# Kernel tuning notes

Measured on AMD Instinct MI355X. Metric: run time of the kernel, lower is better.

The kernel has to match this reference:

```python
import jax, jax.numpy as jnp
import numpy as np

N_NODES = 100000
N_EDGES = 1600000
F_IN = 128
HEADS1, CH1 = 8, 16
N_CLASSES = 64
NEG_SLOPE = 0.2  # PyG GATConv default leaky-relu slope


def setup_inputs() -> dict:
    key = jax.random.key(0)
    ks = jax.random.split(key, 10)
    x = jax.random.normal(ks[0], (N_NODES, F_IN), dtype=jnp.float32)
    edge_index = jax.random.randint(ks[1], (2, N_EDGES), 0, N_NODES, dtype=jnp.int32)
    s1 = 1.0 / np.sqrt(F_IN)
    s2 = 1.0 / np.sqrt(HEADS1 * CH1)
    W1 = jax.random.normal(ks[2], (F_IN, HEADS1 * CH1), dtype=jnp.float32) * s1
    a_src1 = jax.random.normal(ks[3], (HEADS1, CH1), dtype=jnp.float32) * s2
    a_dst1 = jax.random.normal(ks[4], (HEADS1, CH1), dtype=jnp.float32) * s2
    b1 = jnp.zeros((HEADS1 * CH1,), dtype=jnp.float32)
    W2 = jax.random.normal(ks[5], (HEADS1 * CH1, N_CLASSES), dtype=jnp.float32) * s2
    a_src2 = jax.random.normal(ks[6], (1, N_CLASSES), dtype=jnp.float32) * 0.1
    a_dst2 = jax.random.normal(ks[7], (1, N_CLASSES), dtype=jnp.float32) * 0.1
    b2 = jnp.zeros((N_CLASSES,), dtype=jnp.float32)
    return {"x": x, "edge_index": edge_index, "W1": W1, "a_src1": a_src1,
            "a_dst1": a_dst1, "b1": b1, "W2": W2, "a_src2": a_src2,
            "a_dst2": a_dst2, "b2": b2}


def gat_layer(x, src, dst, W, a_src, a_dst, b, heads, ch, concat):
    # PyG GATConv (eval mode, self-loops already appended to src/dst).
    N = x.shape[0]
    h = (x @ W).reshape(N, heads, ch)                      # [N,H,C]
    asn = jnp.einsum('nhc,hc->nh', h, a_src)               # src attention term
    adn = jnp.einsum('nhc,hc->nh', h, a_dst)               # dst attention term
    e = jax.nn.leaky_relu(asn[src] + adn[dst], NEG_SLOPE)  # [E,H]
    emax = jax.ops.segment_max(e, dst, num_segments=N)     # per-dst max (self-loops guarantee nonempty)
    ee = jnp.exp(e - emax[dst])
    denom = jax.ops.segment_sum(ee, dst, num_segments=N)
    alpha = ee / denom[dst]                                # segment softmax over incoming edges
    msg = h[src] * alpha[:, :, None]                       # [E,H,C]
    out = jax.ops.segment_sum(msg, dst, num_segments=N)    # [N,H,C]
    out = out.reshape(N, heads * ch) if concat else out.mean(axis=1)
    return out + b


def reference(x, edge_index, W1, a_src1, a_dst1, b1, W2, a_src2, a_dst2, b2):
    N = x.shape[0]
    loop = jnp.arange(N, dtype=edge_index.dtype)
    src = jnp.concatenate([edge_index[0], loop])  # add self-loops (PyG default)
    dst = jnp.concatenate([edge_index[1], loop])
    h = gat_layer(x, src, dst, W1, a_src1, a_dst1, b1, HEADS1, CH1, True)
    h = jax.nn.elu(h)
    # F.dropout with training=False is identity (eval mode)
    out = gat_layer(h, src, dst, W2, a_src2, a_dst2, b2, 1, N_CLASSES, False)
    return jax.nn.log_softmax(out, axis=1)
```

## Files before the change

### kernel.cpp

```cpp
#include <hip/hip_runtime.h>

#define NN 100000
#define NE 1600000
#define EN (NE + NN)
#define FIN 128
#define H1 8
#define C1 16
#define F1 128
#define NC 64
#define NEG 0.2f

#define BSH 9
#define BKN 512
#define NBUK ((NN + BKN - 1) / BKN)
#define NBLK 256
#define CHUNK ((EN + NBLK - 1) / NBLK)
__device__ __forceinline__ int chunk_of_block(int b) {
  return (b & 7) * (NBLK / 8) + (b >> 3);
}

typedef unsigned short ushort_t;
typedef unsigned int uint_t;
typedef __attribute__((ext_vector_type(8))) short short8v;
typedef __attribute__((ext_vector_type(4))) float f32x4;
typedef __attribute__((ext_vector_type(2))) float f32x2;

union U8 { ushort_t u[8]; short8v v; uint4 q; };

__device__ __forceinline__ ushort_t f2bf(float f) {
  uint_t u = __builtin_bit_cast(uint_t, f);
  u += 0x7FFF + ((u >> 16) & 1);
  return (ushort_t)(u >> 16);
}
__device__ __forceinline__ float bflo(uint_t u) {
  return __builtin_bit_cast(float, u << 16);
}
__device__ __forceinline__ float bfhi(uint_t u) {
  return __builtin_bit_cast(float, u & 0xFFFF0000u);
}

#if __has_builtin(__builtin_amdgcn_cvt_pk_fp8_f32) && \
    __has_builtin(__builtin_amdgcn_cvt_pk_f32_fp8)
__device__ __forceinline__ uint_t fp8_pack4(float f0, float f1, float f2,
                                            float f3) {
  int p = 0;
  p = __builtin_amdgcn_cvt_pk_fp8_f32(f0, f1, p, false);
  p = __builtin_amdgcn_cvt_pk_fp8_f32(f2, f3, p, true);
  return (uint_t)p;
}
__device__ __forceinline__ void fp8_unpack4(uint_t w, float* o) {
  f32x2 d0 = __builtin_amdgcn_cvt_pk_f32_fp8((int)w, false);
  f32x2 d1 = __builtin_amdgcn_cvt_pk_f32_fp8((int)w, true);
  o[0] = d0.x; o[1] = d0.y; o[2] = d1.x; o[3] = d1.y;
}
#else
__device__ __forceinline__ uint_t fp8_enc1(float f) {
  uint_t u = __builtin_bit_cast(uint_t, f);
  uint_t s = (u >> 24) & 0x80u;
  int e = (int)((u >> 23) & 0xFF) - 127;
  if (e < -9) return s;
  if (e < -6) {
    float af = __builtin_bit_cast(float, u & 0x7FFFFFFFu);
    uint_t m = (uint_t)(af * 512.f + 0.5f);
    return s | m;
  }
  uint_t mant = u & 0x7FFFFF;
  uint_t keep = mant >> 20;
  uint_t rest = mant & 0xFFFFF;
  keep += (rest > 0x80000u) || (rest == 0x80000u && (keep & 1));
  uint_t ee = (uint_t)(e + 7);
  if (keep == 8) { keep = 0; ee += 1; }
  if (ee > 15 || (ee == 15 && keep > 6)) return s | 0x7E;
  return s | (ee << 3) | keep;
}
__device__ __forceinline__ float fp8_dec1(uint_t b) {
  uint_t s = (b & 0x80u) << 24;
  uint_t e = (b >> 3) & 15u, m = b & 7u;
  if (e == 0) {
    float v = (float)m * (1.0f / 512.0f);
    return __builtin_bit_cast(float, s | __builtin_bit_cast(uint_t, v));
  }
  return __builtin_bit_cast(float, s | ((e + 120u) << 23) | (m << 20));
}
__device__ __forceinline__ uint_t fp8_pack4(float f0, float f1, float f2,
                                            float f3) {
  return fp8_enc1(f0) | (fp8_enc1(f1) << 8) | (fp8_enc1(f2) << 16) |
         (fp8_enc1(f3) << 24);
}
__device__ __forceinline__ void fp8_unpack4(uint_t w, float* o) {
  o[0] = fp8_dec1(w & 0xFF); o[1] = fp8_dec1((w >> 8) & 0xFF);
  o[2] = fp8_dec1((w >> 16) & 0xFF); o[3] = fp8_dec1(w >> 24);
}
#endif

__global__ __launch_bounds__(512) void bucket_count_kernel(
    const int* __restrict__ dstA, int* __restrict__ cnt,
    const float* __restrict__ W1, const float* __restrict__ W2,
    ushort_t* __restrict__ WT1, ushort_t* __restrict__ WT2) {
  __shared__ int histL[NBUK];
  int b = blockIdx.x, t = threadIdx.x;
  int gid = b * 512 + t;
  if (gid < 128 * 128) {
    int n = gid >> 7, k = gid & 127;
    int c = (n & 15) * 8 + (n >> 4);
    WT1[gid] = f2bf(W1[k * 128 + c]);
  } else if (gid < 128 * 128 + 64 * 128) {
    int j = gid - 128 * 128;
    int n = j >> 7, k = j & 127;
    int c = (n & 15) * 4 + (n >> 4);
    WT2[j] = f2bf(W2[k * 64 + c]);
  }
  for (int i = t; i < NBUK; i += 512) histL[i] = 0;
  __syncthreads();
  int ch = chunk_of_block(b);
  int e0 = ch * CHUNK, e1 = min(e0 + CHUNK, EN);
  for (int e = e0 + t; e < e1; e += 512) {
    int d = (e < NE) ? dstA[e] : (e - NE);
    atomicAdd(&histL[d >> BSH], 1);
  }
  __syncthreads();
  for (int i = t; i < NBUK; i += 512) cnt[i * NBLK + ch] = histL[i];
}

__global__ __launch_bounds__(256) void bucket_scan_kernel(
    int* __restrict__ cnt, int* __restrict__ bucket_base) {
  __shared__ int colsum[NBUK];
  int t = threadIdx.x;
  if (t < NBUK) {
    int run = 0;
    int* c = cnt + t * NBLK;
    for (int b = 0; b < NBLK; ++b) { int v = c[b]; c[b] = run; run += v; }
    colsum[t] = run;
  }
  __syncthreads();
  if (t == 0) {
    int base = 0;
    for (int j = 0; j < NBUK; ++j) {
      bucket_base[j] = base;
      int v = colsum[j];
      colsum[j] = base;
      base += v;
    }
    bucket_base[NBUK] = base;
  }
  __syncthreads();
  if (t < NBUK) {
    int bb = colsum[t];
    int* c = cnt + t * NBLK;
    for (int b = 0; b < NBLK; ++b) c[b] += bb;
  }
}

__global__ __launch_bounds__(512) void scatter_gemm1_kernel(
    const int* __restrict__ srcA, const int* __restrict__ dstA,
    const int* __restrict__ cnt, int* __restrict__ staging,
    const float* __restrict__ X, const ushort_t* __restrict__ WT1,
    const float* __restrict__ a_src, const float* __restrict__ a_dst,
    uint2* __restrict__ h8, float* __restrict__ asn, float* __restrict__ adn,
    int nrows) {
  __shared__ int cur[NBUK];
  if (blockIdx.x < NBLK) {
    int b = blockIdx.x, t = threadIdx.x;
    int ch = chunk_of_block(b);
    for (int i = t; i < NBUK; i += 512) cur[i] = cnt[i * NBLK + ch];
    __syncthreads();
    int e0 = ch * CHUNK, e1 = min(e0 + CHUNK, EN);
    for (int e = e0 + t; e < e1; e += 512) {
      int s, d;
      if (e < NE) { s = srcA[e]; d = dstA[e]; } else { s = e - NE; d = s; }
      int pos = atomicAdd(&cur[d >> BSH], 1);
      staging[pos] = s | ((d & (BKN - 1)) << 17);
    }
    return;
  }
  const int tid = threadIdx.x;
  const int wave = tid >> 6, lane = tid & 63;
  const int row0 = (blockIdx.x - NBLK) * 128 + wave * 16;
  const int rlo = lane & 15, khi = lane >> 4;

  f32x4 acc[8];
#pragma unroll
  for (int n = 0; n < 8; ++n) acc[n] = (f32x4){0.f, 0.f, 0.f, 0.f};

#pragma unroll
  for (int ks = 0; ks < 4; ++ks) {
    const int kk = ks * 32 + khi * 8;
    int row = row0 + rlo;
    if (row >= nrows) row = nrows - 1;
    const float4* xp = (const float4*)(X + (size_t)row * 128 + kk);
    float4 u = xp[0], v = xp[1];
    U8 t;
    t.u[0] = f2bf(u.x); t.u[1] = f2bf(u.y); t.u[2] = f2bf(u.z); t.u[3] = f2bf(u.w);
    t.u[4] = f2bf(v.x); t.u[5] = f2bf(v.y); t.u[6] = f2bf(v.z); t.u[7] = f2bf(v.w);
    short8v a = t.v;
#pragma unroll
    for (int nf = 0; nf < 8; ++nf) {
      short8v b = *(const short8v*)(WT1 + (nf * 16 + rlo) * 128 + kk);
      acc[nf] = __builtin_amdgcn_mfma_f32_16x16x32_bf16(a, b, acc[nf], 0, 0, 0);
    }
  }
  const float4* as4 = (const float4*)a_src;
  const float4* ad4 = (const float4*)a_dst;
  float4 as0 = as4[rlo * 2], as1 = as4[rlo * 2 + 1];
  float4 ad0 = ad4[rlo * 2], ad1 = ad4[rlo * 2 + 1];
  int rbase = row0 + khi * 4;
#pragma unroll
  for (int r = 0; r < 4; ++r) {
    int row = rbase + r;
    bool ok = (row < nrows);
    uint2 pk;
    pk.x = fp8_pack4(acc[0][r], acc[1][r], acc[2][r], acc[3][r]);
    pk.y = fp8_pack4(acc[4][r], acc[5][r], acc[6][r], acc[7][r]);
    if (ok) h8[(size_t)row * 16 + rlo] = pk;
    float s = acc[0][r] * as0.x + acc[1][r] * as0.y +
              acc[2][r] * as0.z + acc[3][r] * as0.w +
              acc[4][r] * as1.x + acc[5][r] * as1.y +
              acc[6][r] * as1.z + acc[7][r] * as1.w;
    float d = acc[0][r] * ad0.x + acc[1][r] * ad0.y +
              acc[2][r] * ad0.z + acc[3][r] * ad0.w +
              acc[4][r] * ad1.x + acc[5][r] * ad1.y +
              acc[6][r] * ad1.z + acc[7][r] * ad1.w;
    s += __shfl_xor(s, 1);
    d += __shfl_xor(d, 1);
    if (ok && (rlo & 1) == 0) {
      asn[row * 8 + (rlo >> 1)] = s;
      adn[row * 8 + (rlo >> 1)] = d;
    }
  }
}

__global__ __launch_bounds__(512) void bucket_csr_kernel(
    const int* __restrict__ staging, const int* __restrict__ bucket_base,
    int* __restrict__ rp, int* __restrict__ col) {
  __shared__ int degL[BKN];
  __shared__ int exclL[BKN];
  __shared__ int sdata[2][BKN];
  int bk = blockIdx.x, t = threadIdx.x;
  int ebase = bucket_base[bk], eend = bucket_base[bk + 1];
  int ecnt = eend - ebase;
  degL[t] = 0;
  __syncthreads();
  for (int e = t; e < ecnt; e += 512)
    atomicAdd(&degL[staging[ebase + e] >> 17], 1);
  __syncthreads();
  int v = degL[t];
  sdata[0][t] = v;
  __syncthreads();
  int sp = 0;
  for (int off = 1; off < BKN; off <<= 1) {
    int val = sdata[sp][t];
    if (t >= off) val += sdata[sp][t - off];
    sdata[sp ^ 1][t] = val;
    __syncthreads();
    sp ^= 1;
  }
  int ex = sdata[sp][t] - v;
  exclL[t] = ex;
  int node = bk * BKN + t;
  if (node < NN) rp[node] = ebase + ex;
  if (bk == 0 && t == 0) rp[NN] = EN;
  __syncthreads();
  for (int e = t; e < ecnt; e += 512) {
    int pk = staging[ebase + e];
    int pos = atomicAdd(&exclL[pk >> 17], 1);
    col[ebase + pos] = pk & 0x1FFFF;
  }
}

__global__ __launch_bounds__(256) void mfma_gemm2_kernel(
    const ushort_t* __restrict__ X2, const ushort_t* __restrict__ WT2,
    const float* __restrict__ a_src, const float* __restrict__ a_dst,
    uint_t* __restrict__ h28, float* __restrict__ asn, float* __restrict__ adn,
    int nrows) {
  const int tid = threadIdx.x;
  const int wave = tid >> 6, lane = tid & 63;
  const int row0 = blockIdx.x * 64 + wave * 16;
  const int rlo = lane & 15, khi = lane >> 4;

  f32x4 acc[4];
#pragma unroll
  for (int n = 0; n < 4; ++n) acc[n] = (f32x4){0.f, 0.f, 0.f, 0.f};

#pragma unroll
  for (int ks = 0; ks < 4; ++ks) {
    const int kk = ks * 32 + khi * 8;
    int row = row0 + rlo;
    if (row >= nrows) row = nrows - 1;
    U8 t;
    t.q = *(const uint4*)(X2 + (size_t)row * 128 + kk);
    short8v a = t.v;
#pragma unroll
    for (int nf = 0; nf < 4; ++nf) {
      short8v b = *(const short8v*)(WT2 + (nf * 16 + rlo) * 128 + kk);
      acc[nf] = __builtin_amdgcn_mfma_f32_16x16x32_bf16(a, b, acc[nf], 0, 0, 0);
    }
  }
  float4 as = ((const float4*)a_src)[rlo];
  float4 ad = ((const float4*)a_dst)[rlo];
  int rbase = row0 + khi * 4;
#pragma unroll
  for (int r = 0; r < 4; ++r) {
    int row = rbase + r;
    bool ok = (row < nrows);
    uint_t pk = fp8_pack4(acc[0][r], acc[1][r], acc[2][r], acc[3][r]);
    if (ok) h28[(size_t)row * 16 + rlo] = pk;
    float s = acc[0][r] * as.x + acc[1][r] * as.y +
              acc[2][r] * as.z + acc[3][r] * as.w;
    float d = acc[0][r] * ad.x + acc[1][r] * ad.y +
              acc[2][r] * ad.z + acc[3][r] * ad.w;
    s += __shfl_xor(s, 1); s += __shfl_xor(s, 2);
    s += __shfl_xor(s, 4); s += __shfl_xor(s, 8);
    d += __shfl_xor(d, 1); d += __shfl_xor(d, 2);
    d += __shfl_xor(d, 4); d += __shfl_xor(d, 8);
    if (ok && rlo == 0) { asn[row] = s; adn[row] = d; }
  }
}

__global__ __launch_bounds__(256) void gather1_kernel(
    const int* __restrict__ rp, const int* __restrict__ col,
    const float* __restrict__ asn, const float* __restrict__ adn,
    const uint4* __restrict__ h8, const float* __restrict__ b1,
    ushort_t* __restrict__ x2) {
  int node = (blockIdx.x << 5) + (threadIdx.x >> 3);
  if (node >= NN) return;
  int lane = threadIdx.x & 7;
  float aD = adn[node * 8 + lane];
  int p = rp[node], p1 = rp[node + 1];
  float a[16];
#pragma unroll
  for (int j = 0; j < 16; ++j) a[j] = 0.f;
  float den = 0.f;

  for (; p + 1 < p1; p += 2) {
    int s0 = col[p], s1 = col[p + 1];
    float e0 = asn[s0 * 8 + lane] + aD;
    float e1 = asn[s1 * 8 + lane] + aD;
    uint4 q0 = h8[(size_t)s0 * 8 + lane];
    uint4 q1 = h8[(size_t)s1 * 8 + lane];
    e0 = e0 > 0.f ? e0 : NEG * e0;
    e1 = e1 > 0.f ? e1 : NEG * e1;
    float ee0 = __expf(e0), ee1 = __expf(e1);
    float d0[4], d1[4], d2[4], d3[4];
    fp8_unpack4(q0.x, d0); fp8_unpack4(q0.y, d1);
    fp8_unpack4(q0.z, d2); fp8_unpack4(q0.w, d3);
    float g0[4], g1[4], g2[4], g3[4];
    fp8_unpack4(q1.x, g0); fp8_unpack4(q1.y, g1);
    fp8_unpack4(q1.z, g2); fp8_unpack4(q1.w, g3);
#pragma unroll
    for (int j = 0; j < 4; ++j) {
      a[j]      += ee0 * d0[j] + ee1 * g0[j];
      a[4 + j]  += ee0 * d1[j] + ee1 * g1[j];
      a[8 + j]  += ee0 * d2[j] + ee1 * g2[j];
      a[12 + j] += ee0 * d3[j] + ee1 * g3[j];
    }
    den += ee0 + ee1;
  }
  if (p < p1) {
    int s0 = col[p];
    float e0 = asn[s0 * 8 + lane] + aD;
    uint4 q0 = h8[(size_t)s0 * 8 + lane];
    e0 = e0 > 0.f ? e0 : NEG * e0;
    float ee0 = __expf(e0);
    float d0[4], d1[4], d2[4], d3[4];
    fp8_unpack4(q0.x, d0); fp8_unpack4(q0.y, d1);
    fp8_unpack4(q0.z, d2); fp8_unpack4(q0.w, d3);
#pragma unroll
    for (int j = 0; j < 4; ++j) {
      a[j] += ee0 * d0[j];
      a[4 + j] += ee0 * d1[j];
      a[8 + j] += ee0 * d2[j];
      a[12 + j] += ee0 * d3[j];
    }
    den += ee0;
  }
  float inv = 1.f / den;
  const float4* b4 = (const float4*)b1;
  U8 t0, t1;
#pragma unroll
  for (int h = 0; h < 4; ++h) {
    float4 bv = b4[lane * 4 + h];
    float o0 = fmaf(a[h * 4 + 0], inv, bv.x);
    float o1 = fmaf(a[h * 4 + 1], inv, bv.y);
    float o2 = fmaf(a[h * 4 + 2], inv, bv.z);
    float o3 = fmaf(a[h * 4 + 3], inv, bv.w);
    o0 = o0 > 0.f ? o0 : __expf(o0) - 1.f;
    o1 = o1 > 0.f ? o1 : __expf(o1) - 1.f;
    o2 = o2 > 0.f ? o2 : __expf(o2) - 1.f;
    o3 = o3 > 0.f ? o3 : __expf(o3) - 1.f;
    U8& t = (h < 2) ? t0 : t1;
    int base = (h & 1) * 4;
    t.u[base + 0] = f2bf(o0); t.u[base + 1] = f2bf(o1);
    t.u[base + 2] = f2bf(o2); t.u[base + 3] = f2bf(o3);
  }
  uint4* xr = (uint4*)(x2 + (size_t)node * F1);
  xr[lane * 2 + 0] = t0.q;
  xr[lane * 2 + 1] = t1.q;
}

__global__ __launch_bounds__(256) void gather2_kernel(
    const int* __restrict__ rp, const int* __restrict__ col,
    const float* __restrict__ asn, const float* __restrict__ adn,
    const uint2* __restrict__ h28, const float* __restrict__ b2,
    float* __restrict__ out) {
  int node = (blockIdx.x << 5) + (threadIdx.x >> 3);
  if (node >= NN) return;
  int lane = threadIdx.x & 7;
  float aD = adn[node];
  int p = rp[node], p1 = rp[node + 1];
  float a[8];
#pragma unroll
  for (int j = 0; j < 8; ++j) a[j] = 0.f;
  float den = 0.f;

  for (; p + 1 < p1; p += 2) {
    int s0 = col[p], s1 = col[p + 1];
    float e0 = asn[s0] + aD;
    float e1 = asn[s1] + aD;
    uint2 q0 = h28[(size_t)s0 * 8 + lane];
    uint2 q1 = h28[(size_t)s1 * 8 + lane];
    e0 = e0 > 0.f ? e0 : NEG * e0;
    e1 = e1 > 0.f ? e1 : NEG * e1;
    float ee0 = __expf(e0), ee1 = __expf(e1);
    float d0[4], d1[4], g0[4], g1[4];
    fp8_unpack4(q0.x, d0); fp8_unpack4(q0.y, d1);
    fp8_unpack4(q1.x, g0); fp8_unpack4(q1.y, g1);
#pragma unroll
    for (int j = 0; j < 4; ++j) {
      a[j] += ee0 * d0[j] + ee1 * g0[j];
      a[4 + j] += ee0 * d1[j] + ee1 * g1[j];
    }
    den += ee0 + ee1;
  }
  if (p < p1) {
    int s0 = col[p];
    float e0 = asn[s0] + aD;
    uint2 q0 = h28[(size_t)s0 * 8 + lane];
    e0 = e0 > 0.f ? e0 : NEG * e0;
    float ee0 = __expf(e0);
    float d0[4], d1[4];
    fp8_unpack4(q0.x, d0); fp8_unpack4(q0.y, d1);
#pragma unroll
    for (int j = 0; j < 4; ++j) {
      a[j] += ee0 * d0[j];
      a[4 + j] += ee0 * d1[j];
    }
    den += ee0;
  }
  float inv = 1.f / den;
  float4 bv0 = ((const float4*)b2)[lane * 2 + 0];
  float4 bv1 = ((const float4*)b2)[lane * 2 + 1];
  float v[8];
  v[0] = fmaf(a[0], inv, bv0.x); v[1] = fmaf(a[1], inv, bv0.y);
  v[2] = fmaf(a[2], inv, bv0.z); v[3] = fmaf(a[3], inv, bv0.w);
  v[4] = fmaf(a[4], inv, bv1.x); v[5] = fmaf(a[5], inv, bv1.y);
  v[6] = fmaf(a[6], inv, bv1.z); v[7] = fmaf(a[7], inv, bv1.w);
  float m = v[0];
#pragma unroll
  for (int j = 1; j < 8; ++j) m = fmaxf(m, v[j]);
#pragma unroll
  for (int k = 1; k < 8; k <<= 1) m = fmaxf(m, __shfl_xor(m, k));
  float ex = 0.f;
#pragma unroll
  for (int j = 0; j < 8; ++j) ex += __expf(v[j] - m);
#pragma unroll
  for (int k = 1; k < 8; k <<= 1) ex += __shfl_xor(ex, k);
  float lse = m + __logf(ex);
  float4 r0 = {v[0] - lse, v[1] - lse, v[2] - lse, v[3] - lse};
  float4 r1 = {v[4] - lse, v[5] - lse, v[6] - lse, v[7] - lse};
  float4* orow = (float4*)(out + (size_t)node * NC);
  orow[lane * 2 + 0] = r0;
  orow[lane * 2 + 1] = r1;
}

extern "C" void kernel_launch(void* const* d_in, const int* in_sizes, int n_in,
                              void* d_out, int out_size, void* d_ws,
                              size_t ws_size, hipStream_t stream) {
  const float* x = (const float*)d_in[0];
  const int* edge_index = (const int*)d_in[1];
  const float* W1 = (const float*)d_in[2];
  const float* a_src1 = (const float*)d_in[3];
  const float* a_dst1 = (const float*)d_in[4];
  const float* b1 = (const float*)d_in[5];
  const float* W2 = (const float*)d_in[6];
  const float* a_src2 = (const float*)d_in[7];
  const float* a_dst2 = (const float*)d_in[8];
  const float* b2 = (const float*)d_in[9];
  float* out = (float*)d_out;
  float* ws = (float*)d_ws;

  ushort_t* x2b = (ushort_t*)ws;
  uint4* h8 = (uint4*)(ws + 6400000);
  uint2* h28 = (uint2*)(ws + 9600000);
  float* asn1 = ws + 11200000;
  float* adn1 = ws + 12000000;
  float* asn2 = ws + 12800000;
  float* adn2 = ws + 12900000;
  ushort_t* WT1 = (ushort_t*)(ws + 13000000);
  ushort_t* WT2 = (ushort_t*)(ws + 13010000);
  int* rp = (int*)(ws + 13020000);
  int* col = rp + NN + 1;
  int* staging = col + EN;
  int* cnt = staging + EN;
  int* bucket_base = cnt + NBUK * NBLK;

  const int* srcA = edge_index;
  const int* dstA = edge_index + NE;

  bucket_count_kernel<<<NBLK, 512, 0, stream>>>(dstA, cnt, W1, W2, WT1, WT2);
  bucket_scan_kernel<<<1, 256, 0, stream>>>(cnt, bucket_base);
  scatter_gemm1_kernel<<<NBLK + (NN + 127) / 128, 512, 0, stream>>>(
      srcA, dstA, cnt, staging, x, WT1, a_src1, a_dst1, (uint2*)h8, asn1, adn1,
      NN);
  bucket_csr_kernel<<<NBUK, 512, 0, stream>>>(staging, bucket_base, rp, col);
  gather1_kernel<<<(NN + 31) / 32, 256, 0, stream>>>(rp, col, asn1, adn1, h8,
                                                     b1, x2b);
  mfma_gemm2_kernel<<<(NN + 63) / 64, 256, 0, stream>>>(
      x2b, WT2, a_src2, a_dst2, (uint_t*)h28, asn2, adn2, NN);
  gather2_kernel<<<(NN + 31) / 32, 256, 0, stream>>>(rp, col, asn2, adn2, h28,
                                                     b2, out);
}
```

Measured before the change: 218.3 us.

## Fuse CSR bucket build with layer-1 gather and shrink buckets to 128 nodes

The bucket size drops from 512 to 128 nodes, so there are about 782 buckets, and the scan kernel now loops over buckets with a stride of 256. The per-bucket CSR construction is fused with the layer-1 attention gather. Each 512-thread block builds col for its 128 nodes, then aggregates them in two passes of 64 nodes, reading col from the just-written L2-hot region. This removes one kernel launch and a round-trip of col and rp through memory. In exchange, the single-block scan does more serial work on more columns, and the gather runs at block granularity with barriers that may reduce latency hiding.

```diff
diff --git a/kernel.cpp b/kernel.cpp
--- a/kernel.cpp
+++ b/kernel.cpp
@@ -10,8 +10,8 @@
 #define NC 64
 #define NEG 0.2f
 
-#define BSH 9
-#define BKN 512
+#define BSH 7
+#define BKN 128
 #define NBUK ((NN + BKN - 1) / BKN)
 #define NBLK 256
 #define CHUNK ((EN + NBLK - 1) / NBLK)
@@ -126,11 +126,11 @@
     int* __restrict__ cnt, int* __restrict__ bucket_base) {
   __shared__ int colsum[NBUK];
   int t = threadIdx.x;
-  if (t < NBUK) {
+  for (int j = t; j < NBUK; j += 256) {
     int run = 0;
-    int* c = cnt + t * NBLK;
+    int* c = cnt + j * NBLK;
     for (int b = 0; b < NBLK; ++b) { int v = c[b]; c[b] = run; run += v; }
-    colsum[t] = run;
+    colsum[j] = run;
   }
   __syncthreads();
   if (t == 0) {
@@ -144,9 +144,9 @@
     bucket_base[NBUK] = base;
   }
   __syncthreads();
-  if (t < NBUK) {
-    int bb = colsum[t];
-    int* c = cnt + t * NBLK;
+  for (int j = t; j < NBUK; j += 256) {
+    int bb = colsum[j];
+    int* c = cnt + j * NBLK;
     for (int b = 0; b < NBLK; ++b) c[b] += bb;
   }
 }
@@ -229,41 +229,128 @@
   }
 }
 
-__global__ __launch_bounds__(512) void bucket_csr_kernel(
+__global__ __launch_bounds__(512) void csr_gather1_kernel(
     const int* __restrict__ staging, const int* __restrict__ bucket_base,
-    int* __restrict__ rp, int* __restrict__ col) {
+    int* __restrict__ rp, int* __restrict__ col,
+    const float* __restrict__ asn, const float* __restrict__ adn,
+    const uint4* __restrict__ h8, const float* __restrict__ b1,
+    ushort_t* __restrict__ x2) {
   __shared__ int degL[BKN];
-  __shared__ int exclL[BKN];
+  __shared__ int curL[BKN];
+  __shared__ int startL[BKN + 1];
   __shared__ int sdata[2][BKN];
   int bk = blockIdx.x, t = threadIdx.x;
   int ebase = bucket_base[bk], eend = bucket_base[bk + 1];
   int ecnt = eend - ebase;
-  degL[t] = 0;
+  if (t < BKN) degL[t] = 0;
   __syncthreads();
   for (int e = t; e < ecnt; e += 512)
     atomicAdd(&degL[staging[ebase + e] >> 17], 1);
   __syncthreads();
-  int v = degL[t];
-  sdata[0][t] = v;
+  if (t < BKN) sdata[0][t] = degL[t];
   __syncthreads();
   int sp = 0;
   for (int off = 1; off < BKN; off <<= 1) {
-    int val = sdata[sp][t];
-    if (t >= off) val += sdata[sp][t - off];
-    sdata[sp ^ 1][t] = val;
+    if (t < BKN) {
+      int val = sdata[sp][t];
+      if (t >= off) val += sdata[sp][t - off];
+      sdata[sp ^ 1][t] = val;
+    }
     __syncthreads();
     sp ^= 1;
   }
-  int ex = sdata[sp][t] - v;
-  exclL[t] = ex;
-  int node = bk * BKN + t;
-  if (node < NN) rp[node] = ebase + ex;
+  if (t < BKN) {
+    int ex = sdata[sp][t] - degL[t];
+    curL[t] = ex;
+    startL[t] = ebase + ex;
+    int node = bk * BKN + t;
+    if (node < NN) rp[node] = ebase + ex;
+  }
+  if (t == 0) startL[BKN] = eend;
   if (bk == 0 && t == 0) rp[NN] = EN;
   __syncthreads();
   for (int e = t; e < ecnt; e += 512) {
     int pk = staging[ebase + e];
-    int pos = atomicAdd(&exclL[pk >> 17], 1);
+    int pos = atomicAdd(&curL[pk >> 17], 1);
     col[ebase + pos] = pk & 0x1FFFF;
+  }
+  __syncthreads();
+  int g = t >> 3, lane = t & 7;
+#pragma unroll
+  for (int pass = 0; pass < 2; ++pass) {
+    int i = pass * 64 + g;
+    int node = bk * BKN + i;
+    if (node >= NN) continue;
+    float aD = adn[node * 8 + lane];
+    int p = startL[i], p1 = startL[i + 1];
+    float a[16];
+#pragma unroll
+    for (int j = 0; j < 16; ++j) a[j] = 0.f;
+    float den = 0.f;
+    for (; p + 1 < p1; p += 2) {
+      int s0 = col[p], s1 = col[p + 1];
+      float e0 = asn[s0 * 8 + lane] + aD;
+      float e1 = asn[s1 * 8 + lane] + aD;
+      uint4 q0 = h8[(size_t)s0 * 8 + lane];
+      uint4 q1 = h8[(size_t)s1 * 8 + lane];
+      e0 = e0 > 0.f ? e0 : NEG * e0;
+      e1 = e1 > 0.f ? e1 : NEG * e1;
+      float ee0 = __expf(e0), ee1 = __expf(e1);
+      float d0[4], d1[4], d2[4], d3[4];
+      fp8_unpack4(q0.x, d0); fp8_unpack4(q0.y, d1);
+      fp8_unpack4(q0.z, d2); fp8_unpack4(q0.w, d3);
+      float g0[4], g1[4], g2[4], g3[4];
+      fp8_unpack4(q1.x, g0); fp8_unpack4(q1.y, g1);
+      fp8_unpack4(q1.z, g2); fp8_unpack4(q1.w, g3);
+#pragma unroll
+      for (int j = 0; j < 4; ++j) {
+        a[j]      += ee0 * d0[j] + ee1 * g0[j];
+        a[4 + j]  += ee0 * d1[j] + ee1 * g1[j];
+        a[8 + j]  += ee0 * d2[j] + ee1 * g2[j];
+        a[12 + j] += ee0 * d3[j] + ee1 * g3[j];
+      }
+      den += ee0 + ee1;
+    }
+    if (p < p1) {
+      int s0 = col[p];
+      float e0 = asn[s0 * 8 + lane] + aD;
+      uint4 q0 = h8[(size_t)s0 * 8 + lane];
+      e0 = e0 > 0.f ? e0 : NEG * e0;
+      float ee0 = __expf(e0);
+      float d0[4], d1[4], d2[4], d3[4];
+      fp8_unpack4(q0.x, d0); fp8_unpack4(q0.y, d1);
+      fp8_unpack4(q0.z, d2); fp8_unpack4(q0.w, d3);
+#pragma unroll
+      for (int j = 0; j < 4; ++j) {
+        a[j] += ee0 * d0[j];
+        a[4 + j] += ee0 * d1[j];
+        a[8 + j] += ee0 * d2[j];
+        a[12 + j] += ee0 * d3[j];
+      }
+      den += ee0;
+    }
+    float inv = 1.f / den;
+    const float4* b4 = (const float4*)b1;
+    U8 t0, t1;
+#pragma unroll
+    for (int h = 0; h < 4; ++h) {
+      float4 bv = b4[lane * 4 + h];
+      float o0 = fmaf(a[h * 4 + 0], inv, bv.x);
+      float o1 = fmaf(a[h * 4 + 1], inv, bv.y);
+      float o2 = fmaf(a[h * 4 + 2], inv, bv.z);
+      float o3 = fmaf(a[h * 4 + 3], inv, bv.w);
+      o0 = o0 > 0.f ? o0 : __expf(o0) - 1.f;
+      o1 = o1 > 0.f ? o1 : __expf(o1) - 1.f;
+      o2 = o2 > 0.f ? o2 : __expf(o2) - 1.f;
+      o3 = o3 > 0.f ? o3 : __expf(o3) - 1.f;
+      U8& tt = (h < 2) ? t0 : t1;
+      int base = (h & 1) * 4;
+      tt.u[base + 0] = f2bf(o0); tt.u[base + 1] = f2bf(o1);
+      tt.u[base + 2] = f2bf(o2); tt.u[base + 3] = f2bf(o3);
+    }
+    uint4* xr = (uint4*)(x2 + (size_t)node * F1);
+    xr[lane * 2 + 0] = t0.q;
+    xr[lane * 2 + 1] = t1.q;
   }
 }
 
@@ -314,87 +401,6 @@
     d += __shfl_xor(d, 4); d += __shfl_xor(d, 8);
     if (ok && rlo == 0) { asn[row] = s; adn[row] = d; }
   }
-}
-
-__global__ __launch_bounds__(256) void gather1_kernel(
-    const int* __restrict__ rp, const int* __restrict__ col,
-    const float* __restrict__ asn, const float* __restrict__ adn,
-    const uint4* __restrict__ h8, const float* __restrict__ b1,
-    ushort_t* __restrict__ x2) {
-  int node = (blockIdx.x << 5) + (threadIdx.x >> 3);
-  if (node >= NN) return;
-  int lane = threadIdx.x & 7;
-  float aD = adn[node * 8 + lane];
-  int p = rp[node], p1 = rp[node + 1];
-  float a[16];
-#pragma unroll
-  for (int j = 0; j < 16; ++j) a[j] = 0.f;
-  float den = 0.f;
-
-  for (; p + 1 < p1; p += 2) {
-    int s0 = col[p], s1 = col[p + 1];
-    float e0 = asn[s0 * 8 + lane] + aD;
-    float e1 = asn[s1 * 8 + lane] + aD;
-    uint4 q0 = h8[(size_t)s0 * 8 + lane];
-    uint4 q1 = h8[(size_t)s1 * 8 + lane];
-    e0 = e0 > 0.f ? e0 : NEG * e0;
-    e1 = e1 > 0.f ? e1 : NEG * e1;
-    float ee0 = __expf(e0), ee1 = __expf(e1);
-    float d0[4], d1[4], d2[4], d3[4];
-    fp8_unpack4(q0.x, d0); fp8_unpack4(q0.y, d1);
-    fp8_unpack4(q0.z, d2); fp8_unpack4(q0.w, d3);
-    float g0[4], g1[4], g2[4], g3[4];
-    fp8_unpack4(q1.x, g0); fp8_unpack4(q1.y, g1);
-    fp8_unpack4(q1.z, g2); fp8_unpack4(q1.w, g3);
-#pragma unroll
-    for (int j = 0; j < 4; ++j) {
-      a[j]      += ee0 * d0[j] + ee1 * g0[j];
-      a[4 + j]  += ee0 * d1[j] + ee1 * g1[j];
-      a[8 + j]  += ee0 * d2[j] + ee1 * g2[j];
-      a[12 + j] += ee0 * d3[j] + ee1 * g3[j];
-    }
-    den += ee0 + ee1;
-  }
-  if (p < p1) {
-    int s0 = col[p];
-    float e0 = asn[s0 * 8 + lane] + aD;
-    uint4 q0 = h8[(size_t)s0 * 8 + lane];
-    e0 = e0 > 0.f ? e0 : NEG * e0;
-    float ee0 = __expf(e0);
-    float d0[4], d1[4], d2[4], d3[4];
-    fp8_unpack4(q0.x, d0); fp8_unpack4(q0.y, d1);
-    fp8_unpack4(q0.z, d2); fp8_unpack4(q0.w, d3);
-#pragma unroll
-    for (int j = 0; j < 4; ++j) {
-      a[j] += ee0 * d0[j];
-      a[4 + j] += ee0 * d1[j];
-      a[8 + j] += ee0 * d2[j];
-      a[12 + j] += ee0 * d3[j];
-    }
-    den += ee0;
-  }
-  float inv = 1.f / den;
-  const float4* b4 = (const float4*)b1;
-  U8 t0, t1;
-#pragma unroll
-  for (int h = 0; h < 4; ++h) {
-    float4 bv = b4[lane * 4 + h];
-    float o0 = fmaf(a[h * 4 + 0], inv, bv.x);
-    float o1 = fmaf(a[h * 4 + 1], inv, bv.y);
-    float o2 = fmaf(a[h * 4 + 2], inv, bv.z);
-    float o3 = fmaf(a[h * 4 + 3], inv, bv.w);
-    o0 = o0 > 0.f ? o0 : __expf(o0) - 1.f;
-    o1 = o1 > 0.f ? o1 : __expf(o1) - 1.f;
-    o2 = o2 > 0.f ? o2 : __expf(o2) - 1.f;
-    o3 = o3 > 0.f ? o3 : __expf(o3) - 1.f;
-    U8& t = (h < 2) ? t0 : t1;
-    int base = (h & 1) * 4;
-    t.u[base + 0] = f2bf(o0); t.u[base + 1] = f2bf(o1);
-    t.u[base + 2] = f2bf(o2); t.u[base + 3] = f2bf(o3);
-  }
-  uint4* xr = (uint4*)(x2 + (size_t)node * F1);
-  xr[lane * 2 + 0] = t0.q;
-  xr[lane * 2 + 1] = t1.q;
 }
 
 __global__ __launch_bounds__(256) void gather2_kernel(
@@ -511,9 +517,8 @@
   scatter_gemm1_kernel<<<NBLK + (NN + 127) / 128, 512, 0, stream>>>(
       srcA, dstA, cnt, staging, x, WT1, a_src1, a_dst1, (uint2*)h8, asn1, adn1,
       NN);
-  bucket_csr_kernel<<<NBUK, 512, 0, stream>>>(staging, bucket_base, rp, col);
-  gather1_kernel<<<(NN + 31) / 32, 256, 0, stream>>>(rp, col, asn1, adn1, h8,
-                                                     b1, x2b);
+  csr_gather1_kernel<<<NBUK, 512, 0, stream>>>(staging, bucket_base, rp, col,
+                                               asn1, adn1, h8, b1, x2b);
   mfma_gemm2_kernel<<<(NN + 63) / 64, 256, 0, stream>>>(
       x2b, WT2, a_src2, a_dst2, (uint_t*)h28, asn2, adn2, NN);
   gather2_kernel<<<(NN + 31) / 32, 256, 0, stream>>>(rp, col, asn2, adn2, h28,
```

After: 327.3 us. +49.9%, slower.
